# Kernel tuning notes

Hardware: AMD Instinct MI355X
Metric: run time of the kernel (lower is better)

The kernel has to match this reference:

```python
import jax, jax.numpy as jnp
import numpy as np

S = 512      # seq_length (fixed by generate_mask(m=512, n=512))
B = 16       # batch
H = 1024     # hidden_size
N = 16       # num_attention_heads
HD = H // N  # hidden per head = 64
DENSITY = 0.1  # sparsity = 0.9


def setup_inputs() -> dict:
    key = jax.random.key(0)
    k0, k1, k2, k3 = jax.random.split(key, 4)
    hidden_states = jax.random.normal(k0, (S, B, H), dtype=jnp.float32)
    attention_mask = jax.random.uniform(k1, (S, S)) < DENSITY
    attention_mask = attention_mask | jnp.eye(S, dtype=bool)  # no empty rows
    scale = 1.0 / np.sqrt(H).astype(np.float32)
    Wqkv = jax.random.normal(k2, (H, 3 * H), dtype=jnp.float32) * scale
    bqkv = jnp.zeros((3 * H,), dtype=jnp.float32)
    Wout = jax.random.normal(k3, (H, H), dtype=jnp.float32) * scale
    bout = jnp.zeros((H,), dtype=jnp.float32)
    return {"hidden_states": hidden_states, "attention_mask": attention_mask,
            "Wqkv": Wqkv, "bqkv": bqkv, "Wout": Wout, "bout": bout}


def reference(hidden_states, attention_mask, Wqkv, bqkv, Wout, bout):
    # hidden_states: [s, b, h] -> [b, s, h]
    x = jnp.transpose(hidden_states, (1, 0, 2))
    b = x.shape[0]
    # fused QKV projection, then per-head split of the last dim into (q,k,v) chunks
    qkv = (x @ Wqkv + bqkv).reshape(b, S, N, 3 * HD)
    q, k, v = qkv[..., :HD], qkv[..., HD:2 * HD], qkv[..., 2 * HD:]  # [b, s, n, hd]
    # SDDMM: scores only meaningful on mask nonzeros (dense-masked equivalent)
    scores = jnp.einsum('bind,bjnd->bnij', q, k) / np.sqrt(HD).astype(np.float32)
    neg = jnp.finfo(scores.dtype).min
    scores = jnp.where(attention_mask, scores, neg)
    # CSR softmax: softmax over the nonzeros of each row
    weights = jax.nn.softmax(scores, axis=-1)
    weights = jnp.where(attention_mask, weights, jnp.zeros((), scores.dtype))
    # SpMM: sparse weights @ dense values
    ctx = jnp.einsum('bnij,bjnd->bind', weights, v)  # [b, s, n, hd]
    # [b, s, n, hd] -> [s, b, n*hd]
    context = jnp.transpose(ctx, (1, 0, 2, 3)).reshape(S, b, H)
    return context @ Wout + bout  # [s, b, h]
```

## Files before the change

kernel.cpp:

```cpp
#include <hip/hip_runtime.h>
#include <hip/hip_bf16.h>

typedef __hip_bfloat16 bf16;
typedef unsigned short u16;
typedef unsigned int u32;
typedef unsigned long long u64;
typedef float f32x4 __attribute__((ext_vector_type(4)));
typedef short s16x8 __attribute__((ext_vector_type(8)));
typedef unsigned short u16x4 __attribute__((ext_vector_type(4)));

static constexpr int SQ    = 512;
static constexpr int BB    = 16;
static constexpr int HH    = 1024;
static constexpr int NHEAD = 16;
static constexpr int ROWS  = SQ * BB;
static constexpr int QKVC  = 3 * HH;

static constexpr long long OFF_FLAGS = 0;
static constexpr long long OFF_M16   = 4096;
static constexpr long long OFF_WQT   = 1048576;
static constexpr long long OFF_WOT   = OFF_WQT + (long long)QKVC * HH * 2;
static constexpr long long OFF_QK    = OFF_WOT + (long long)HH * HH * 2;
static constexpr long long OFF_VT    = OFF_QK + (long long)ROWS * 2048 * 2;
static constexpr long long OFF_CTX   = OFF_VT + (long long)256 * 64 * 512 * 2;

__device__ __forceinline__ float load_f(const void* p, long long i, int is_bf16) {
  if (is_bf16) return __bfloat162float(((const bf16*)p)[i]);
  return ((const float*)p)[i];
}
__device__ __forceinline__ u16 f2b(float x) { bf16 h = __float2bfloat16(x); return *(u16*)&h; }
__device__ __forceinline__ f32x4 mfma_bf16(s16x8 a, s16x8 b, f32x4 c) {
  return __builtin_amdgcn_mfma_f32_16x16x32_bf16(a, b, c, 0, 0, 0);
}
__device__ __forceinline__ void gll16(const void* g, void* lds) {
  __builtin_amdgcn_global_load_lds((const __attribute__((address_space(1))) unsigned int*)g,
                                   (__attribute__((address_space(3))) unsigned int*)lds, 16, 0, 0);
}
__device__ __forceinline__ u32 cvtpk(float lo, float hi) {
  u32 r;
  asm volatile("v_cvt_pk_bf16_f32 %0, %1, %2" : "=v"(r) : "v"(lo), "v"(hi));
  return r;
}
__device__ __forceinline__ void xcd_swz(int& bx, int& by) {
  int gx = gridDim.x;
  int nw = gx * gridDim.y;
  int lin = by * gx + bx;
  int q = nw >> 3;
  int nl = (lin & 7) * q + (lin >> 3);
  bx = nl % gx;
  by = nl / gx;
}

__global__ __launch_bounds__(256) void sa_detect_part(const void* hs, const void* mask, int* cnt) {
  __shared__ int lc[6];
  if (threadIdx.x < 6) lc[threadIdx.x] = 0;
  __syncthreads();
  int gid = blockIdx.x * 256 + threadIdx.x;
  if (gid < 2048) {
    unsigned short v = ((const unsigned short*)hs)[2 * gid];
    float f = __uint_as_float(((unsigned)v) << 16);
    float a = fabsf(f);
    if (v == 0 || (a > 1e-9f && a < 1e4f)) atomicAdd(&lc[0], 1);
  }
  const unsigned char* mb = (const unsigned char*)mask;
  int codd = 0, c1 = 0, c3f = 0, c48 = 0, cb1 = 0;
  #pragma unroll
  for (int r = 0; r < 4; ++r) {
    int i = gid * 4 + r;
    int base = i * 4;
    unsigned char b1 = mb[base + 1], b3 = mb[base + 3];
    if (b1 | b3) codd++;
    if (b1) cb1++;
    if (b1 == 1) c1++;
    if (b3 == 1) c1++;
    if (b1 == 0x3f) c3f++;
    if (b3 == 0x3f) c3f++;
    if (i & 1) { if (mb[base]) c48++; }
  }
  atomicAdd(&lc[1], codd);
  atomicAdd(&lc[2], c1);
  atomicAdd(&lc[3], c3f);
  atomicAdd(&lc[4], c48);
  atomicAdd(&lc[5], cb1);
  __syncthreads();
  if (threadIdx.x < 6) atomicAdd(&cnt[threadIdx.x], lc[threadIdx.x]);
}

__global__ void sa_detect_fin(const int* cnt, int* flags) {
  if (threadIdx.x != 0) return;
  flags[0] = (cnt[0] > 1800) ? 1 : 0;
  int mm;
  if (cnt[1] == 0)           mm = (cnt[4] > 0) ? 0 : 1;
  else if (cnt[2] >= cnt[3]) mm = 2;
  else if (cnt[5] == 0)      mm = 3;
  else                       mm = 4;
  flags[1] = mm;
}

__global__ __launch_bounds__(256) void sa_maskexp(const void* mask, u16* m16, const int* flags) {
  int idx = blockIdx.x * 256 + threadIdx.x;
  int i = idx >> 9, c = idx & 511;
  int jw = c >> 5, r = c & 31;
  int g = r >> 3, q = r & 7;
  int t = q >> 2, rr = q & 3;
  long long j = (long long)i * 512 + jw * 32 + t * 16 + 4 * g + rr;
  int mm = flags[1];
  bool v;
  if      (mm == 0) v = ((const int*)mask)[j] != 0;
  else if (mm == 1) v = ((const long long*)mask)[j] != 0;
  else if (mm == 2) v = ((const unsigned char*)mask)[j] != 0;
  else if (mm == 3) v = ((const float*)mask)[j] != 0.0f;
  else              v = ((const unsigned short*)mask)[j] != 0;
  m16[idx] = v ? 0xFFFFu : 0u;
}

__global__ __launch_bounds__(256) void sa_cvt_hs(const void* hs, u16* hsb, const int* flags) {
  if (flags[0]) return;
  int tid = blockIdx.x * 256 + threadIdx.x;
  int row = tid >> 7, u7 = tid & 127;
  int sc = u7 >> 3, u = u7 & 7;
  long long ebase = (long long)row * 1024 + sc * 64 + u * 8;
  const float4* pf = (const float4*)((const float*)hs + ebase);
  float4 x0 = pf[0], x1 = pf[1];
  s16x8 ov;
  ov[0] = f2b(x0.x); ov[1] = f2b(x0.y); ov[2] = f2b(x0.z); ov[3] = f2b(x0.w);
  ov[4] = f2b(x1.x); ov[5] = f2b(x1.y); ov[6] = f2b(x1.z); ov[7] = f2b(x1.w);
  *(s16x8*)((char*)hsb + (long long)row * 2048 + sc * 128 + ((u ^ (row & 7)) * 16)) = ov;
}

__global__ __launch_bounds__(256) void sa_wtransc(const void* W, u16* WT, int Nld, const int* flags) {
  int nrow = blockIdx.x * 256 + threadIdx.x;
  int sc = blockIdx.y >> 3, u = blockIdx.y & 7;
  int kb = sc * 64 + u * 8;
  const int fl = flags[0];
  s16x8 ov;
  #pragma unroll
  for (int e = 0; e < 8; ++e) ov[e] = f2b(load_f(W, (long long)(kb + e) * Nld + nrow, fl));
  *(s16x8*)((char*)WT + (long long)nrow * 2048 + sc * 128 + ((u ^ (nrow & 7)) * 16)) = ov;
}

__global__ __launch_bounds__(256) void mm_qkv(const u16* __restrict__ hs, const u16* __restrict__ hsb,
                                              const u16* __restrict__ BT, const void* bias,
                                              u16* qk, u16* V, const int* flags) {
  __shared__ u16 As[128 * 64];
  __shared__ u16 Bs[128 * 64];
  const int tid = threadIdx.x, w = tid >> 6, lane = tid & 63;
  const int g = lane >> 4, li = lane & 15;
  int bx = blockIdx.x, by = blockIdx.y;
  xcd_swz(bx, by);
  const int m0 = by * 128, n0 = bx * 128;
  const int wm = (w >> 1) * 64, wn = (w & 1) * 64;
  const int K = 1024;
  const int fl = flags[0];
  f32x4 acc[4][4] = {};
  for (int k0 = 0; k0 < K; k0 += 64) {
    if (k0) __syncthreads();
    #pragma unroll
    for (int q = 0; q < 4; ++q) {
      int c = w * 4 + q;
      int r = c * 8 + (lane >> 3);
      const u16* asrc = fl ? (hs  + (long long)(m0 + r) * K + k0 + (((lane & 7) ^ (r & 7)) * 8))
                           : (hsb + (long long)(m0 + r) * K + k0 + ((lane & 7) * 8));
      gll16(asrc, &As[c * 512]);
      gll16(BT + (long long)(n0 + r) * K + k0 + (lane & 7) * 8, &Bs[c * 512]);
    }
    __syncthreads();
    #pragma unroll
    for (int ks = 0; ks < 2; ++ks) {
      s16x8 af[4], bfr[4];
      #pragma unroll
      for (int mi = 0; mi < 4; ++mi) {
        int r = wm + mi * 16 + li;
        int off = (ks * 64 + g * 16) ^ ((r & 7) << 4);
        af[mi] = *(const s16x8*)((const char*)As + r * 128 + off);
      }
      #pragma unroll
      for (int nj = 0; nj < 4; ++nj) {
        int r = wn + nj * 16 + li;
        int off = (ks * 64 + g * 16) ^ ((r & 7) << 4);
        bfr[nj] = *(const s16x8*)((const char*)Bs + r * 128 + off);
      }
      #pragma unroll
      for (int mi = 0; mi < 4; ++mi)
        #pragma unroll
        for (int nj = 0; nj < 4; ++nj)
          acc[mi][nj] = mfma_bf16(af[mi], bfr[nj], acc[mi][nj]);
    }
  }
  const int s0 = (m0 + wm) >> 4;
  #pragma unroll
  for (int nj = 0; nj < 4; ++nj) {
    int colbase = n0 + wn + nj * 16;
    int col = colbase + li;
    float bv = load_f(bias, col, fl);
    int c16 = colbase >> 4;
    int ht = c16 % 12, n = c16 / 12;
    int colmod = (ht * 16) + li;
    if (ht < 8) {
      #pragma unroll
      for (int mi = 0; mi < 4; ++mi) {
        int s = s0 + mi;
        #pragma unroll
        for (int rr = 0; rr < 4; ++rr) {
          int b = 4 * g + rr;
          qk[((long long)(b * 512 + s)) * 2048 + n * 128 + colmod] =
              f2b(acc[mi][nj][rr] + bv);
        }
      }
    } else {
      int d = colmod - 128;
      #pragma unroll
      for (int rr = 0; rr < 4; ++rr) {
        int b = 4 * g + rr;
        #pragma unroll
        for (int mi = 0; mi < 4; ++mi)
          V[((long long)(b * 16 + n)) * 32768 + (s0 + mi) * 64 + d] =
              f2b(acc[mi][nj][rr] + bv);
      }
    }
  }
}

__global__ __launch_bounds__(1024) void sa_attn5(const u16* __restrict__ qk, const u16* __restrict__ V,
                                                 const u16* __restrict__ m16, u16* __restrict__ ctx) {
  __shared__ __align__(16) u16 SHM[49152];
  u16* const Vs = SHM;
  u16* const PB = SHM + 32768;

  const int tid = threadIdx.x, w = tid >> 6, lane = tid & 63;
  const int g = lane >> 4, li = lane & 15;
  const int n = blockIdx.x, b = blockIdx.y;

  const u16* vg = V + (long long)(b * 16 + n) * 32768;
  #pragma unroll
  for (int q = 0; q < 4; ++q) {
    int lin = q * 1024 + tid;
    int s = lin >> 3, dc = lin & 7;
    s16x8 v = *(const s16x8*)(vg + s * 64 + dc * 8);
    #pragma unroll
    for (int e = 0; e < 8; ++e) {
      int d = dc * 8 + e;
      Vs[d * 512 + (((s >> 3) ^ e ^ dc) * 8) + (s & 7)] = v[e];
    }
  }
  __syncthreads();

  const int i0 = w * 32;
  s16x8 qf0[2], qf1[2];
  #pragma unroll
  for (int tl = 0; tl < 2; ++tl) {
    const u16* qb = qk + ((long long)(b * 512 + i0 + tl * 16 + li)) * 2048 + n * 128;
    qf0[tl] = *(const s16x8*)(qb + g * 8);
    qf1[tl] = *(const s16x8*)(qb + 32 + g * 8);
  }
  s16x8 af1;
  #pragma unroll
  for (int e = 0; e < 8; ++e) af1[e] = (li == 0) ? (short)0x3F80 : (short)0;

  char* const pw = (char*)PB + w * 2048;
  const float SC  = 0.125f * 1.44269504f;
  const float THR = 44.3614f;

  const u16* kbase = qk + (long long)(b * 512) * 2048 + n * 128 + 64;
  const u16* mk0 = m16 + (long long)(i0 + li) * 512 + g * 8;
  const u16* mk1 = m16 + (long long)(i0 + 16 + li) * 512 + g * 8;

  f32x4 cacc[2][4] = {};
  f32x4 lacc[2] = {};
  float m[2] = {-1e30f, -1e30f};

  for (int jw = 0; jw < 16; ++jw) {
    uint4 mmv[2];
    mmv[0] = *(const uint4*)(mk0 + jw * 32);
    mmv[1] = *(const uint4*)(mk1 + jw * 32);
    s16x8 kf0[2], kf1[2];
    #pragma unroll
    for (int t = 0; t < 2; ++t) {
      const u16* kb = kbase + (long long)(jw * 32 + t * 16 + li) * 2048;
      kf0[t] = *(const s16x8*)(kb + g * 8);
      kf1[t] = *(const s16x8*)(kb + 32 + g * 8);
    }
    f32x4 sa[2][2];
    #pragma unroll
    for (int tl = 0; tl < 2; ++tl)
      #pragma unroll
      for (int t = 0; t < 2; ++t) {
        f32x4 z = {};
        z = mfma_bf16(kf0[t], qf0[tl], z);
        z = mfma_bf16(kf1[t], qf1[tl], z);
        sa[tl][t] = z;
      }
    s16x8 pf[2];
    #pragma unroll
    for (int tl = 0; tl < 2; ++tl) {
      float pm = fmaxf(fmaxf(fmaxf(sa[tl][0][0], sa[tl][0][1]), fmaxf(sa[tl][0][2], sa[tl][0][3])),
                       fmaxf(fmaxf(sa[tl][1][0], sa[tl][1][1]), fmaxf(sa[tl][1][2], sa[tl][1][3])));
      pm = fmaxf(pm, __shfl_xor(pm, 16));
      pm = fmaxf(pm, __shfl_xor(pm, 32));
      if (__any(pm > m[tl] + THR)) {
        float mn = fmaxf(m[tl], pm);
        float sc = __builtin_exp2f((m[tl] - mn) * SC);
        lacc[tl] *= sc;
        #pragma unroll
        for (int dt = 0; dt < 4; ++dt) cacc[tl][dt] *= sc;
        m[tl] = mn;
      }
      float mv = m[tl];
      float p0 = __builtin_exp2f((sa[tl][0][0] - mv) * SC);
      float p1 = __builtin_exp2f((sa[tl][0][1] - mv) * SC);
      float p2 = __builtin_exp2f((sa[tl][0][2] - mv) * SC);
      float p3 = __builtin_exp2f((sa[tl][0][3] - mv) * SC);
      float p4 = __builtin_exp2f((sa[tl][1][0] - mv) * SC);
      float p5 = __builtin_exp2f((sa[tl][1][1] - mv) * SC);
      float p6 = __builtin_exp2f((sa[tl][1][2] - mv) * SC);
      float p7 = __builtin_exp2f((sa[tl][1][3] - mv) * SC);
      u32 r0 = cvtpk(p0, p1) & mmv[tl].x;
      u32 r1 = cvtpk(p2, p3) & mmv[tl].y;
      u32 r2 = cvtpk(p4, p5) & mmv[tl].z;
      u32 r3 = cvtpk(p6, p7) & mmv[tl].w;
      char* pt = pw + tl * 1024 + li * 64;
      *(uint2*)(pt + ((g ^ (li & 6)) * 8))       = make_uint2(r0, r1);
      *(uint2*)(pt + (((4 + g) ^ (li & 6)) * 8)) = make_uint2(r2, r3);
      pf[tl] = *(const s16x8*)(pw + tl * 1024 + li * 64 + (((2 * g) ^ (li & 6)) * 8));
      lacc[tl] = mfma_bf16(af1, pf[tl], lacc[tl]);
    }
    #pragma unroll
    for (int dt = 0; dt < 4; ++dt) {
      int d = dt * 16 + li;
      s16x8 vf = *(const s16x8*)(Vs + d * 512 +
                                 (((jw * 4 + g) ^ (d & 7) ^ ((d >> 3) & 7)) * 8));
      #pragma unroll
      for (int tl = 0; tl < 2; ++tl)
        cacc[tl][dt] = mfma_bf16(vf, pf[tl], cacc[tl][dt]);
    }
  }
  #pragma unroll
  for (int tl = 0; tl < 2; ++tl) {
    float lv = __shfl(lacc[tl][0], li);
    float inv = 1.0f / lv;
    #pragma unroll
    for (int dt = 0; dt < 4; ++dt) {
      u32 lo = cvtpk(cacc[tl][dt][0] * inv, cacc[tl][dt][1] * inv);
      u32 hi = cvtpk(cacc[tl][dt][2] * inv, cacc[tl][dt][3] * inv);
      *(uint2*)(pw + li * 128 + (((dt * 4 + g) ^ ((li & 7) << 1)) * 8)) = make_uint2(lo, hi);
    }
    int il = lane >> 2;
    #pragma unroll
    for (int p = 0; p < 2; ++p) {
      int c = (lane & 3) + p * 4;
      s16x8 v = *(const s16x8*)(pw + il * 128 + (((2 * c) ^ ((il & 7) << 1)) * 8));
      *(s16x8*)(ctx + ((long long)((i0 + tl * 16 + il) * 16 + b)) * 1024 + n * 64 +
                ((c ^ (b & 7)) * 8)) = v;
    }
  }
}

__global__ __launch_bounds__(256) void mm_out(const u16* __restrict__ Asrc, const u16* __restrict__ BT,
                                              const void* bias, void* out, const int* flags) {
  __shared__ u16 As[128 * 64];
  __shared__ u16 Bs[128 * 64];
  const int tid = threadIdx.x, w = tid >> 6, lane = tid & 63;
  const int g = lane >> 4, li = lane & 15;
  int bx = blockIdx.x, by = blockIdx.y;
  xcd_swz(bx, by);
  const int m0 = by * 128, n0 = bx * 128;
  const int wm = (w >> 1) * 64, wn = (w & 1) * 64;
  const int K = 1024;
  f32x4 acc[4][4] = {};
  for (int k0 = 0; k0 < K; k0 += 64) {
    if (k0) __syncthreads();
    #pragma unroll
    for (int q = 0; q < 4; ++q) {
      int c = w * 4 + q;
      int r = c * 8 + (lane >> 3);
      gll16(Asrc + (long long)(m0 + r) * K + k0 + (lane & 7) * 8, &As[c * 512]);
      gll16(BT   + (long long)(n0 + r) * K + k0 + (lane & 7) * 8, &Bs[c * 512]);
    }
    __syncthreads();
    #pragma unroll
    for (int ks = 0; ks < 2; ++ks) {
      s16x8 af[4], bfr[4];
      #pragma unroll
      for (int mi = 0; mi < 4; ++mi) {
        int r = wm + mi * 16 + li;
        int off = (ks * 64 + g * 16) ^ ((r & 7) << 4);
        af[mi] = *(const s16x8*)((const char*)As + r * 128 + off);
      }
      #pragma unroll
      for (int nj = 0; nj < 4; ++nj) {
        int r = wn + nj * 16 + li;
        int off = (ks * 64 + g * 16) ^ ((r & 7) << 4);
        bfr[nj] = *(const s16x8*)((const char*)Bs + r * 128 + off);
      }
      #pragma unroll
      for (int mi = 0; mi < 4; ++mi)
        #pragma unroll
        for (int nj = 0; nj < 4; ++nj)
          acc[mi][nj] = mfma_bf16(af[mi], bfr[nj], acc[mi][nj]);
    }
  }
  const int fl = flags[0];
  #pragma unroll
  for (int nj = 0; nj < 4; ++nj) {
    int col = n0 + wn + nj * 16 + li;
    float bv = load_f(bias, col, fl);
    #pragma unroll
    for (int mi = 0; mi < 4; ++mi) {
      #pragma unroll
      for (int rr = 0; rr < 4; ++rr) {
        long long row = m0 + wm + mi * 16 + 4 * g + rr;
        float v = acc[mi][nj][rr] + bv;
        if (fl) ((u16*)out)[row * 1024 + col] = f2b(v);
        else    ((float*)out)[row * 1024 + col] = v;
      }
    }
  }
}

extern "C" void kernel_launch(void* const* d_in, const int* in_sizes, int n_in,
                              void* d_out, int out_size, void* d_ws, size_t ws_size,
                              hipStream_t stream) {
  const void* hs   = d_in[0];
  const void* mask = d_in[1];
  const void* Wqkv = d_in[2];
  const void* bqkv = d_in[3];
  const void* Wout = d_in[4];
  const void* bout = d_in[5];

  char* ws = (char*)d_ws;
  int* flags = (int*)(ws + OFF_FLAGS);
  int* cnt   = (int*)(ws + 64);
  u16* m16   = (u16*)(ws + OFF_M16);
  u16* WqkvT = (u16*)(ws + OFF_WQT);
  u16* WoutT = (u16*)(ws + OFF_WOT);
  u16* qk    = (u16*)(ws + OFF_QK);
  u16* V     = (u16*)(ws + OFF_VT);
  u16* ctx   = (u16*)(ws + OFF_CTX);
  u16* hsb   = ctx;

  hipMemsetAsync(cnt, 0, 64, stream);
  sa_detect_part<<<64, 256, 0, stream>>>(hs, mask, cnt);
  sa_detect_fin<<<1, 64, 0, stream>>>(cnt, flags);
  sa_maskexp<<<1024, 256, 0, stream>>>(mask, m16, flags);
  sa_cvt_hs<<<(ROWS * 128) / 256, 256, 0, stream>>>(hs, hsb, flags);
  sa_wtransc<<<dim3(QKVC / 256, 128), 256, 0, stream>>>(Wqkv, WqkvT, QKVC, flags);
  sa_wtransc<<<dim3(HH / 256, 128), 256, 0, stream>>>(Wout, WoutT, HH, flags);

  mm_qkv<<<dim3(QKVC / 128, ROWS / 128), 256, 0, stream>>>(
      (const u16*)hs, hsb, WqkvT, bqkv, qk, V, flags);
  sa_attn5<<<dim3(NHEAD, BB), 1024, 0, stream>>>(qk, V, m16, ctx);
  mm_out<<<dim3(HH / 128, ROWS / 128), 256, 0, stream>>>(ctx, WoutT, bout, d_out, flags);
}
```

Baseline: 194.1 us.

## Stage K tile in LDS for attention and merge setup kernel launches

Removes the separate flag-finalizing kernel; each consumer now derives the dtype and mask-mode flags directly from the detection counters. The two weight-transpose launches are merged into one 3D grid, with out-of-range blocks for the smaller matrix exiting early. In the attention kernel, the per-head K slice is preloaded into swizzled shared memory so K fragments come from LDS instead of strided global reads. The price is more LDS per block (160KB), which limits occupancy to one block per CU, plus redundant counter reads in every kernel.

```diff
diff --git a/kernel.cpp b/kernel.cpp
--- a/kernel.cpp
+++ b/kernel.cpp
@@ -49,6 +49,13 @@
   int nl = (lin & 7) * q + (lin >> 3);
   bx = nl % gx;
   by = nl / gx;
+}
+__device__ __forceinline__ int fl_from(const int* cnt) { return cnt[0] > 1800 ? 1 : 0; }
+__device__ __forceinline__ int mm_from(const int* cnt) {
+  if (cnt[1] == 0)      return (cnt[4] > 0) ? 0 : 1;
+  if (cnt[2] >= cnt[3]) return 2;
+  if (cnt[5] == 0)      return 3;
+  return 4;
 }
 
 __global__ __launch_bounds__(256) void sa_detect_part(const void* hs, const void* mask, int* cnt) {
@@ -86,25 +93,14 @@
   if (threadIdx.x < 6) atomicAdd(&cnt[threadIdx.x], lc[threadIdx.x]);
 }
 
-__global__ void sa_detect_fin(const int* cnt, int* flags) {
-  if (threadIdx.x != 0) return;
-  flags[0] = (cnt[0] > 1800) ? 1 : 0;
-  int mm;
-  if (cnt[1] == 0)           mm = (cnt[4] > 0) ? 0 : 1;
-  else if (cnt[2] >= cnt[3]) mm = 2;
-  else if (cnt[5] == 0)      mm = 3;
-  else                       mm = 4;
-  flags[1] = mm;
-}
-
-__global__ __launch_bounds__(256) void sa_maskexp(const void* mask, u16* m16, const int* flags) {
+__global__ __launch_bounds__(256) void sa_maskexp(const void* mask, u16* m16, const int* cnt) {
   int idx = blockIdx.x * 256 + threadIdx.x;
   int i = idx >> 9, c = idx & 511;
   int jw = c >> 5, r = c & 31;
   int g = r >> 3, q = r & 7;
   int t = q >> 2, rr = q & 3;
   long long j = (long long)i * 512 + jw * 32 + t * 16 + 4 * g + rr;
-  int mm = flags[1];
+  int mm = mm_from(cnt);
   bool v;
   if      (mm == 0) v = ((const int*)mask)[j] != 0;
   else if (mm == 1) v = ((const long long*)mask)[j] != 0;
@@ -114,8 +110,8 @@
   m16[idx] = v ? 0xFFFFu : 0u;
 }
 
-__global__ __launch_bounds__(256) void sa_cvt_hs(const void* hs, u16* hsb, const int* flags) {
-  if (flags[0]) return;
+__global__ __launch_bounds__(256) void sa_cvt_hs(const void* hs, u16* hsb, const int* cnt) {
+  if (fl_from(cnt)) return;
   int tid = blockIdx.x * 256 + threadIdx.x;
   int row = tid >> 7, u7 = tid & 127;
   int sc = u7 >> 3, u = u7 & 7;
@@ -128,11 +124,15 @@
   *(s16x8*)((char*)hsb + (long long)row * 2048 + sc * 128 + ((u ^ (row & 7)) * 16)) = ov;
 }
 
-__global__ __launch_bounds__(256) void sa_wtransc(const void* W, u16* WT, int Nld, const int* flags) {
+__global__ __launch_bounds__(256) void sa_wtransc2(const void* Wq, u16* WqT, const void* Wo, u16* WoT,
+                                                   const int* cnt) {
+  const void* W; u16* WT; int Nld;
+  if (blockIdx.z == 0) { W = Wq; WT = WqT; Nld = QKVC; }
+  else                 { if (blockIdx.x >= HH / 256) return; W = Wo; WT = WoT; Nld = HH; }
   int nrow = blockIdx.x * 256 + threadIdx.x;
   int sc = blockIdx.y >> 3, u = blockIdx.y & 7;
   int kb = sc * 64 + u * 8;
-  const int fl = flags[0];
+  const int fl = fl_from(cnt);
   s16x8 ov;
   #pragma unroll
   for (int e = 0; e < 8; ++e) ov[e] = f2b(load_f(W, (long long)(kb + e) * Nld + nrow, fl));
@@ -141,7 +141,7 @@
 
 __global__ __launch_bounds__(256) void mm_qkv(const u16* __restrict__ hs, const u16* __restrict__ hsb,
                                               const u16* __restrict__ BT, const void* bias,
-                                              u16* qk, u16* V, const int* flags) {
+                                              u16* qk, u16* V, const int* cnt) {
   __shared__ u16 As[128 * 64];
   __shared__ u16 Bs[128 * 64];
   const int tid = threadIdx.x, w = tid >> 6, lane = tid & 63;
@@ -151,7 +151,7 @@
   const int m0 = by * 128, n0 = bx * 128;
   const int wm = (w >> 1) * 64, wn = (w & 1) * 64;
   const int K = 1024;
-  const int fl = flags[0];
+  const int fl = fl_from(cnt);
   f32x4 acc[4][4] = {};
   for (int k0 = 0; k0 < K; k0 += 64) {
     if (k0) __syncthreads();
@@ -221,16 +221,25 @@
   }
 }
 
-__global__ __launch_bounds__(1024) void sa_attn5(const u16* __restrict__ qk, const u16* __restrict__ V,
+__global__ __launch_bounds__(1024) void sa_attn7(const u16* __restrict__ qk, const u16* __restrict__ V,
                                                  const u16* __restrict__ m16, u16* __restrict__ ctx) {
-  __shared__ __align__(16) u16 SHM[49152];
-  u16* const Vs = SHM;
-  u16* const PB = SHM + 32768;
+  __shared__ __align__(16) u16 SHM[81920];
+  u16* const Ks = SHM;
+  u16* const Vs = SHM + 32768;
+  u16* const PB = SHM + 65536;
 
   const int tid = threadIdx.x, w = tid >> 6, lane = tid & 63;
   const int g = lane >> 4, li = lane & 15;
   const int n = blockIdx.x, b = blockIdx.y;
 
+  const u16* kg = qk + (long long)(b * 512) * 2048 + n * 128 + 64;
+  #pragma unroll
+  for (int it = 0; it < 4; ++it) {
+    int lin = it * 1024 + tid;
+    int s = lin >> 3, c = lin & 7;
+    s16x8 kv = *(const s16x8*)(kg + (long long)s * 2048 + c * 8);
+    *(s16x8*)(Ks + s * 64 + ((c ^ (s & 7)) * 8)) = kv;
+  }
   const u16* vg = V + (long long)(b * 16 + n) * 32768;
   #pragma unroll
   for (int q = 0; q < 4; ++q) {
@@ -261,7 +270,6 @@
   const float SC  = 0.125f * 1.44269504f;
   const float THR = 44.3614f;
 
-  const u16* kbase = qk + (long long)(b * 512) * 2048 + n * 128 + 64;
   const u16* mk0 = m16 + (long long)(i0 + li) * 512 + g * 8;
   const u16* mk1 = m16 + (long long)(i0 + 16 + li) * 512 + g * 8;
 
@@ -276,9 +284,10 @@
     s16x8 kf0[2], kf1[2];
     #pragma unroll
     for (int t = 0; t < 2; ++t) {
-      const u16* kb = kbase + (long long)(jw * 32 + t * 16 + li) * 2048;
-      kf0[t] = *(const s16x8*)(kb + g * 8);
-      kf1[t] = *(const s16x8*)(kb + 32 + g * 8);
+      int j = jw * 32 + t * 16 + li;
+      const u16* kb = Ks + j * 64;
+      kf0[t] = *(const s16x8*)(kb + ((g ^ (j & 7)) * 8));
+      kf1[t] = *(const s16x8*)(kb + (((4 + g) ^ (j & 7)) * 8));
     }
     f32x4 sa[2][2];
     #pragma unroll
@@ -356,7 +365,7 @@
 }
 
 __global__ __launch_bounds__(256) void mm_out(const u16* __restrict__ Asrc, const u16* __restrict__ BT,
-                                              const void* bias, void* out, const int* flags) {
+                                              const void* bias, void* out, const int* cnt) {
   __shared__ u16 As[128 * 64];
   __shared__ u16 Bs[128 * 64];
   const int tid = threadIdx.x, w = tid >> 6, lane = tid & 63;
@@ -399,7 +408,7 @@
           acc[mi][nj] = mfma_bf16(af[mi], bfr[nj], acc[mi][nj]);
     }
   }
-  const int fl = flags[0];
+  const int fl = fl_from(cnt);
   #pragma unroll
   for (int nj = 0; nj < 4; ++nj) {
     int col = n0 + wn + nj * 16 + li;
@@ -428,7 +437,6 @@
   const void* bout = d_in[5];
 
   char* ws = (char*)d_ws;
-  int* flags = (int*)(ws + OFF_FLAGS);
   int* cnt   = (int*)(ws + 64);
   u16* m16   = (u16*)(ws + OFF_M16);
   u16* WqkvT = (u16*)(ws + OFF_WQT);
@@ -440,14 +448,12 @@
 
   hipMemsetAsync(cnt, 0, 64, stream);
   sa_detect_part<<<64, 256, 0, stream>>>(hs, mask, cnt);
-  sa_detect_fin<<<1, 64, 0, stream>>>(cnt, flags);
-  sa_maskexp<<<1024, 256, 0, stream>>>(mask, m16, flags);
-  sa_cvt_hs<<<(ROWS * 128) / 256, 256, 0, stream>>>(hs, hsb, flags);
-  sa_wtransc<<<dim3(QKVC / 256, 128), 256, 0, stream>>>(Wqkv, WqkvT, QKVC, flags);
-  sa_wtransc<<<dim3(HH / 256, 128), 256, 0, stream>>>(Wout, WoutT, HH, flags);
+  sa_maskexp<<<1024, 256, 0, stream>>>(mask, m16, cnt);
+  sa_cvt_hs<<<(ROWS * 128) / 256, 256, 0, stream>>>(hs, hsb, cnt);
+  sa_wtransc2<<<dim3(QKVC / 256, 128, 2), 256, 0, stream>>>(Wqkv, WqkvT, Wout, WoutT, cnt);
 
   mm_qkv<<<dim3(QKVC / 128, ROWS / 128), 256, 0, stream>>>(
-      (const u16*)hs, hsb, WqkvT, bqkv, qk, V, flags);
-  sa_attn5<<<dim3(NHEAD, BB), 1024, 0, stream>>>(qk, V, m16, ctx);
-  mm_out<<<dim3(HH / 128, ROWS / 128), 256, 0, stream>>>(ctx, WoutT, bout, d_out, flags);
-}
+      (const u16*)hs, hsb, WqkvT, bqkv, qk, V, cnt);
+  sa_attn7<<<dim3(NHEAD, BB), 1024, 0, stream>>>(qk, V, m16, ctx);
+  mm_out<<<dim3(HH / 128, ROWS / 128), 256, 0, stream>>>(ctx, WoutT, bout, d_out, cnt);
+}
```

After: 177.5 us. -8.5%, faster.
